# Kernel optimization log

Measured on AMD Instinct MI355X. Metric: run time of the kernel, lower is better.

Reference implementation:

```python
import jax, jax.numpy as jnp
import numpy as np

EPS = 0.5  # diffusion epsilon from init_kwargs

def setup_inputs() -> dict:
    key = jax.random.key(0)
    k = jax.random.split(key, 7)
    B, N0, N1, n = 1024, 32, 32, 64
    Mu0 = jax.random.normal(k[0], (N0, n), dtype=jnp.float32) * 2.0
    Mu1 = jax.random.normal(k[1], (N1, n), dtype=jnp.float32) * 2.0
    # diagonal covariances must be positive
    S0 = jax.random.uniform(k[2], (N0, n), dtype=jnp.float32, minval=0.1, maxval=1.0)
    S1 = jax.random.uniform(k[3], (N1, n), dtype=jnp.float32, minval=0.1, maxval=1.0)
    Lam = jax.random.uniform(k[4], (N0, N1), dtype=jnp.float32, minval=0.0, maxval=1.0)
    Lam = Lam / Lam.sum()  # transport plan sums to 1
    X = jax.random.normal(k[5], (B, n), dtype=jnp.float32)
    t = jnp.float32(0.3)
    return {"X": X, "Mu0": Mu0, "Mu1": Mu1, "S0": S0, "S1": S1, "Lam": Lam, "t": t}

def reference(X, Mu0, Mu1, S0, S1, Lam, t):
    eps2 = EPS * EPS
    S0e = S0[:, None, :]        # (N0,1,n)
    S1e = S1[None, :, :]        # (1,N1,n)
    Ds = jnp.sqrt(4.0 * S0e * S1e + EPS ** 4)
    Cs = 0.5 * (Ds - eps2)                       # (N0,N1,n)
    mu_t = (1.0 - t) * Mu0[:, None, :] + t * Mu1[None, :, :]  # (N0,N1,n)
    Sigma = (1.0 - t) ** 2 * S0e + t ** 2 * S1e + 2.0 * t * (1.0 - t) * (Cs + 0.5 * eps2)
    # St = Pt - Qt - eps^2 * t
    St = t * S1e + (1.0 - t) * Cs - ((1.0 - t) * S0e + t * Cs) - eps2 * t
    K = St / Sigma                               # (N0,N1,n)
    v = Mu1[None, :, :] - Mu0[:, None, :]        # (N0,N1,n)
    d = X[:, None, None, :] - mu_t               # (B,N0,N1,n)
    U = K * d + v                                # (B,N0,N1,n)
    # diag-Normal log_prob plus n/2*log(2pi) == -0.5*sum(d^2/Sigma + log Sigma)
    logw = -0.5 * jnp.sum(d * d / Sigma + jnp.log(Sigma), axis=-1)  # (B,N0,N1)
    W = jnp.exp(jnp.clip(logw, -50.0, 50.0)) * Lam                  # (B,N0,N1)
    num = jnp.einsum('bijn,bij->bn', U, W)       # (B,n)
    den = jnp.sum(W, axis=(1, 2))[:, None]       # (B,1)
    return num / den
```

## Files before the change

### kernel.cpp

```cpp
#include <hip/hip_runtime.h>
#include <math.h>

#define EPS2f 0.25f
#define EPS4f 0.0625f

__global__ __launch_bounds__(256) void precomp_kernel(
    const float* __restrict__ Mu0, const float* __restrict__ Mu1,
    const float* __restrict__ S0,  const float* __restrict__ S1,
    const float* __restrict__ tptr,
    float2* __restrict__ AB2, float2* __restrict__ KV2,
    float* __restrict__ C0)
{
    const int tid = threadIdx.x;
    const int k   = tid & 63;
    const int ij  = (blockIdx.x << 2) + (tid >> 6);
    const int i   = ij >> 5;
    const int j   = ij & 31;
    const float t   = *tptr;
    const float omt = 1.0f - t;

    const float s0 = S0[i * 64 + k];
    const float s1 = S1[j * 64 + k];
    const float m0 = Mu0[i * 64 + k];
    const float m1 = Mu1[j * 64 + k];

    const float ds  = sqrtf(4.0f * s0 * s1 + EPS4f);
    const float cs  = 0.5f * (ds - EPS2f);
    const float mt  = omt * m0 + t * m1;
    const float sig = omt * omt * s0 + t * t * s1
                    + 2.0f * t * omt * (cs + 0.5f * EPS2f);
    const float isig = 1.0f / sig;
    const float st = t * s1 - omt * s0 + (omt - t) * cs - EPS2f * t;
    const float kk = st * isig;
    const float v  = m1 - m0;

    AB2[((k >> 1) << 11) + (ij << 1) + (k & 1)] = make_float2(isig, 2.0f * mt * isig);
    KV2[((ij >> 1) << 7) + (k << 1) + (ij & 1)] = make_float2(kk, v - kk * mt);

    float c = mt * mt * isig + __logf(sig);
    #pragma unroll
    for (int off = 32; off >= 1; off >>= 1)
        c += __shfl_xor(c, off, 64);
    if (k == 0) C0[ij] = c;
}

__global__ __launch_bounds__(1024) void gmm_main_kernel(
    const float* __restrict__ X,   const float* __restrict__ Lam,
    const float* __restrict__ C0,
    const float4* __restrict__ AB4, const float4* __restrict__ KV4,
    float* __restrict__ out)
{
    __shared__ float4 Xs4[64];
    __shared__ float4 Wl4[1024 * 2];
    __shared__ float  red[16 * 64 * 5];
    __shared__ float  XsT[4 * 64];
    __shared__ float  denp[16 * 4];

    const int tid  = threadIdx.x;
    const int lane = tid & 63;
    const int w    = tid >> 6;
    const int b0   = blockIdx.x << 2;

    if (tid < 256) {
        const int bb = tid >> 6, k = tid & 63;
        const float xv = X[(b0 + bb) * 64 + k];
        ((float*)&Xs4[k])[bb] = xv;
        XsT[bb * 64 + k] = xv;
    }
    __syncthreads();

    const int ij = tid;
    const float c0 = C0[ij];
    const float lm = Lam[ij];
    float qa = 0.f, qb = 0.f, qc = 0.f, qd = 0.f;
    #pragma unroll 8
    for (int k2 = 0; k2 < 32; ++k2) {
        const float4 ab = AB4[(k2 << 10) + ij];
        const float4 x0 = Xs4[2 * k2];
        const float4 x1 = Xs4[2 * k2 + 1];
        qa = fmaf(fmaf(ab.x, x0.x, -ab.y), x0.x, qa);
        qb = fmaf(fmaf(ab.x, x0.y, -ab.y), x0.y, qb);
        qc = fmaf(fmaf(ab.x, x0.z, -ab.y), x0.z, qc);
        qd = fmaf(fmaf(ab.x, x0.w, -ab.y), x0.w, qd);
        qa = fmaf(fmaf(ab.z, x1.x, -ab.w), x1.x, qa);
        qb = fmaf(fmaf(ab.z, x1.y, -ab.w), x1.y, qb);
        qc = fmaf(fmaf(ab.z, x1.z, -ab.w), x1.z, qc);
        qd = fmaf(fmaf(ab.z, x1.w, -ab.w), x1.w, qd);
    }

    #define WCALC(q) (__expf(fminf(fmaxf(-0.5f * ((q) + c0), -50.f), 50.f)) * lm)
    float4 wv4;
    wv4.x = WCALC(qa); wv4.y = WCALC(qb); wv4.z = WCALC(qc); wv4.w = WCALC(qd);
    #undef WCALC
    Wl4[ij * 2] = wv4;

    float d0 = wv4.x, d1 = wv4.y, d2 = wv4.z, d3 = wv4.w;
    #pragma unroll
    for (int off = 32; off >= 1; off >>= 1) {
        d0 += __shfl_xor(d0, off, 64);
        d1 += __shfl_xor(d1, off, 64);
        d2 += __shfl_xor(d2, off, 64);
        d3 += __shfl_xor(d3, off, 64);
    }
    if (lane == 0) {
        denp[w * 4 + 0] = d0; denp[w * 4 + 1] = d1;
        denp[w * 4 + 2] = d2; denp[w * 4 + 3] = d3;
    }

    const float xk0 = XsT[0 * 64 + lane], xk1 = XsT[1 * 64 + lane];
    const float xk2 = XsT[2 * 64 + lane], xk3 = XsT[3 * 64 + lane];
    float n0 = 0.f, n1 = 0.f, n2 = 0.f, n3 = 0.f;
    const int p0 = w << 5;
    #pragma unroll 8
    for (int p = 0; p < 32; ++p) {
        const float4 kv = KV4[((p0 + p) << 6) + lane];
        const float4 we = Wl4[(p0 + p) * 4];
        const float4 wo = Wl4[(p0 + p) * 4 + 2];
        float u;
        u = fmaf(kv.x, xk0, kv.y); n0 = fmaf(we.x, u, n0);
        u = fmaf(kv.x, xk1, kv.y); n1 = fmaf(we.y, u, n1);
        u = fmaf(kv.x, xk2, kv.y); n2 = fmaf(we.z, u, n2);
        u = fmaf(kv.x, xk3, kv.y); n3 = fmaf(we.w, u, n3);
        u = fmaf(kv.z, xk0, kv.w); n0 = fmaf(wo.x, u, n0);
        u = fmaf(kv.z, xk1, kv.w); n1 = fmaf(wo.y, u, n1);
        u = fmaf(kv.z, xk2, kv.w); n2 = fmaf(wo.z, u, n2);
        u = fmaf(kv.z, xk3, kv.w); n3 = fmaf(wo.w, u, n3);
    }
    {
        float* r = &red[(w * 64 + lane) * 5];
        r[0] = n0; r[1] = n1; r[2] = n2; r[3] = n3;
    }
    __syncthreads();

    if (tid < 256) {
        const int bb = tid >> 6, k = tid & 63;
        float s = 0.f, d = 0.f;
        #pragma unroll
        for (int ww = 0; ww < 16; ++ww) {
            s += red[(ww * 64 + k) * 5 + bb];
            d += denp[ww * 4 + bb];
        }
        out[(b0 + bb) * 64 + k] = s / d;
    }
}

extern "C" void kernel_launch(void* const* d_in, const int* in_sizes, int n_in,
                              void* d_out, int out_size, void* d_ws, size_t ws_size,
                              hipStream_t stream) {
    const float* X   = (const float*)d_in[0];
    const float* Mu0 = (const float*)d_in[1];
    const float* Mu1 = (const float*)d_in[2];
    const float* S0  = (const float*)d_in[3];
    const float* S1  = (const float*)d_in[4];
    const float* Lam = (const float*)d_in[5];
    const float* t   = (const float*)d_in[6];
    float* out = (float*)d_out;

    char* ws = (char*)d_ws;
    float2* AB2 = (float2*)(ws);
    float2* KV2 = (float2*)(ws + (512 << 10));
    float*  C0  = (float*)(ws + (1024 << 10));

    precomp_kernel<<<256, 256, 0, stream>>>(Mu0, Mu1, S0, S1, t, AB2, KV2, C0);
    gmm_main_kernel<<<256, 1024, 0, stream>>>(X, Lam, C0,
                                              (const float4*)AB2,
                                              (const float4*)KV2, out);
}
```

Baseline: 77.79 us.

## Stage precompute stores through LDS and software-prefetch AB/KV in main kernel

```diff
diff --git a/kernel.cpp b/kernel.cpp
--- a/kernel.cpp
+++ b/kernel.cpp
@@ -11,9 +11,14 @@
     float2* __restrict__ AB2, float2* __restrict__ KV2,
     float* __restrict__ C0)
 {
+    __shared__ float2 abS[4][67];
+    __shared__ float2 kvS[4][64];
+
     const int tid = threadIdx.x;
     const int k   = tid & 63;
-    const int ij  = (blockIdx.x << 2) + (tid >> 6);
+    const int ijl = tid >> 6;
+    const int ij0 = blockIdx.x << 2;
+    const int ij  = ij0 + ijl;
     const int i   = ij >> 5;
     const int j   = ij & 31;
     const float t   = *tptr;
@@ -34,14 +39,29 @@
     const float kk = st * isig;
     const float v  = m1 - m0;
 
-    AB2[((k >> 1) << 11) + (ij << 1) + (k & 1)] = make_float2(isig, 2.0f * mt * isig);
-    KV2[((ij >> 1) << 7) + (k << 1) + (ij & 1)] = make_float2(kk, v - kk * mt);
+    abS[ijl][k] = make_float2(isig, 2.0f * mt * isig);
+    kvS[ijl][k] = make_float2(kk, v - kk * mt);
 
     float c = mt * mt * isig + __logf(sig);
     #pragma unroll
     for (int off = 32; off >= 1; off >>= 1)
         c += __shfl_xor(c, off, 64);
     if (k == 0) C0[ij] = c;
+
+    __syncthreads();
+
+    {
+        const int k2   = tid >> 3;
+        const int ijl2 = (tid >> 1) & 3;
+        const int par  = tid & 1;
+        AB2[(k2 << 11) + ((ij0 + ijl2) << 1) + par] = abS[ijl2][2 * k2 + par];
+    }
+    {
+        const int pr  = tid >> 7;
+        const int k6  = (tid >> 1) & 63;
+        const int par = tid & 1;
+        KV2[(blockIdx.x << 8) + tid] = kvS[(pr << 1) + par][k6];
+    }
 }
 
 __global__ __launch_bounds__(1024) void gmm_main_kernel(
@@ -67,25 +87,33 @@
         ((float*)&Xs4[k])[bb] = xv;
         XsT[bb * 64 + k] = xv;
     }
-    __syncthreads();
 
     const int ij = tid;
+    const float4* __restrict__ abp = AB4 + ij;
     const float c0 = C0[ij];
     const float lm = Lam[ij];
+
+    float4 ab[8];
+    #pragma unroll
+    for (int g = 0; g < 8; ++g) ab[g] = abp[g << 10];
+
+    __syncthreads();
+
     float qa = 0.f, qb = 0.f, qc = 0.f, qd = 0.f;
-    #pragma unroll 8
+    #pragma unroll
     for (int k2 = 0; k2 < 32; ++k2) {
-        const float4 ab = AB4[(k2 << 10) + ij];
+        const float4 a = ab[k2 & 7];
+        if (k2 + 8 < 32) ab[k2 & 7] = abp[(k2 + 8) << 10];
         const float4 x0 = Xs4[2 * k2];
         const float4 x1 = Xs4[2 * k2 + 1];
-        qa = fmaf(fmaf(ab.x, x0.x, -ab.y), x0.x, qa);
-        qb = fmaf(fmaf(ab.x, x0.y, -ab.y), x0.y, qb);
-        qc = fmaf(fmaf(ab.x, x0.z, -ab.y), x0.z, qc);
-        qd = fmaf(fmaf(ab.x, x0.w, -ab.y), x0.w, qd);
-        qa = fmaf(fmaf(ab.z, x1.x, -ab.w), x1.x, qa);
-        qb = fmaf(fmaf(ab.z, x1.y, -ab.w), x1.y, qb);
-        qc = fmaf(fmaf(ab.z, x1.z, -ab.w), x1.z, qc);
-        qd = fmaf(fmaf(ab.z, x1.w, -ab.w), x1.w, qd);
+        qa = fmaf(fmaf(a.x, x0.x, -a.y), x0.x, qa);
+        qb = fmaf(fmaf(a.x, x0.y, -a.y), x0.y, qb);
+        qc = fmaf(fmaf(a.x, x0.z, -a.y), x0.z, qc);
+        qd = fmaf(fmaf(a.x, x0.w, -a.y), x0.w, qd);
+        qa = fmaf(fmaf(a.z, x1.x, -a.w), x1.x, qa);
+        qb = fmaf(fmaf(a.z, x1.y, -a.w), x1.y, qb);
+        qc = fmaf(fmaf(a.z, x1.z, -a.w), x1.z, qc);
+        qd = fmaf(fmaf(a.z, x1.w, -a.w), x1.w, qd);
     }
 
     #define WCALC(q) (__expf(fminf(fmaxf(-0.5f * ((q) + c0), -50.f), 50.f)) * lm)
@@ -94,6 +122,13 @@
     #undef WCALC
     Wl4[ij * 2] = wv4;
 
+    const int p0 = w << 5;
+    float4 kvb[8];
+    #pragma unroll
+    for (int q = 0; q < 8; ++q) kvb[q] = KV4[((p0 + q) << 6) + lane];
+    const float xk0 = XsT[0 * 64 + lane], xk1 = XsT[1 * 64 + lane];
+    const float xk2 = XsT[2 * 64 + lane], xk3 = XsT[3 * 64 + lane];
+
     float d0 = wv4.x, d1 = wv4.y, d2 = wv4.z, d3 = wv4.w;
     #pragma unroll
     for (int off = 32; off >= 1; off >>= 1) {
@@ -107,13 +142,11 @@
         denp[w * 4 + 2] = d2; denp[w * 4 + 3] = d3;
     }
 
-    const float xk0 = XsT[0 * 64 + lane], xk1 = XsT[1 * 64 + lane];
-    const float xk2 = XsT[2 * 64 + lane], xk3 = XsT[3 * 64 + lane];
     float n0 = 0.f, n1 = 0.f, n2 = 0.f, n3 = 0.f;
-    const int p0 = w << 5;
-    #pragma unroll 8
+    #pragma unroll
     for (int p = 0; p < 32; ++p) {
-        const float4 kv = KV4[((p0 + p) << 6) + lane];
+        const float4 kv = kvb[p & 7];
+        if (p + 8 < 32) kvb[p & 7] = KV4[((p0 + p + 8) << 6) + lane];
         const float4 we = Wl4[(p0 + p) * 4];
         const float4 wo = Wl4[(p0 + p) * 4 + 2];
         float u;
```

Result: no change. 77.53 us (-0.3%).
